# Optimization experiments

Measured on AMD Instinct MI355X. Metric: run time of the kernel, lower is better.

Reference implementation:

```python
import jax, jax.numpy as jnp
import numpy as np

N, K, CIN, COUT = 150000, 27, 128, 128


def setup_inputs() -> dict:
    key = jax.random.key(0)
    k1, k2, k3 = jax.random.split(key, 3)
    data = jax.random.normal(k1, (N, CIN), dtype=jnp.float32)
    weights = jax.random.normal(k2, (COUT, K, CIN), dtype=jnp.float32) * 0.05
    # neighbour indices in [-1, N): -1 marks empty octree neighbours (~1/151 here)
    neighbour = jax.random.randint(k3, (N, K), 0, N + 1, dtype=jnp.int64) - 1
    return {"data": data, "weights": weights, "neighbour": neighbour}


def reference(data, weights, neighbour):
    """Octree sparse conv: out[m] = sum_k W[:,k,:] @ data[neigh[m,k]] (0 if -1).

    Scans over the 27 kernel offsets so the [N,K,Cin] gather is never
    materialized; each step is a masked row-gather + dense GEMM.
    """
    w_k = jnp.transpose(weights, (1, 2, 0))   # [K, Cin, Cout]
    n_k = neighbour.T                          # [K, N]

    def body(acc, xs):
        w, idx = xs                            # [Cin, Cout], [N]
        valid = (idx >= 0)[:, None]            # [N, 1]
        g = jnp.where(valid, data[jnp.clip(idx, 0, None)], 0.0)  # [N, Cin]
        return acc + g @ w, None

    out0 = jnp.zeros((data.shape[0], w_k.shape[-1]), dtype=data.dtype)
    out, _ = jax.lax.scan(body, out0, (w_k, n_k))
    return out
```

## Files before the change

kernel.cpp:

```cpp
#include <hip/hip_runtime.h>

#define N_PTS 150000
#define NK 27
#define CIN 128
#define COUT 128
#define BM 128
#define NBLK ((N_PTS + BM - 1) / BM)

typedef __attribute__((ext_vector_type(8))) short bfrag8;
typedef __attribute__((ext_vector_type(4))) float facc4;

__device__ inline unsigned short f2bf(float f) {
    unsigned u = __builtin_bit_cast(unsigned, f);
    u += 0x7FFFu + ((u >> 16) & 1u);
    return (unsigned short)(u >> 16);
}
__device__ inline unsigned pack2(float a, float b) {
    return (unsigned)f2bf(a) | ((unsigned)f2bf(b) << 16);
}
__device__ inline void glds16(const void* g, void* l) {
    __builtin_amdgcn_global_load_lds(
        (const __attribute__((address_space(1))) void*)g,
        (__attribute__((address_space(3))) void*)l, 16, 0, 0);
}

__global__ void cast_data_kernel(const float* __restrict__ in,
                                 unsigned short* __restrict__ out) {
    const int n8_data = N_PTS * (CIN / 8);
    const int n8_all  = (N_PTS + 1) * (CIN / 8);
    int i = blockIdx.x * blockDim.x + threadIdx.x;
    int stride = gridDim.x * blockDim.x;
    for (; i < n8_all; i += stride) {
        uint4 v;
        if (i < n8_data) {
            const float4* p = (const float4*)(in + (size_t)i * 8);
            float4 x = p[0], y = p[1];
            v.x = pack2(x.x, x.y); v.y = pack2(x.z, x.w);
            v.z = pack2(y.x, y.y); v.w = pack2(y.z, y.w);
        } else {
            v.x = v.y = v.z = v.w = 0u;
        }
        *(uint4*)(out + (size_t)i * 8) = v;
    }
}

__global__ void prep_weights_h(const float* __restrict__ w,
                               unsigned short* __restrict__ wkh) {
    int i = blockIdx.x * blockDim.x + threadIdx.x;
    if (i >= NK * 2 * 128 * 8) return;
    int bu = i & 7, co = (i >> 3) & 127, h = (i >> 10) & 1, k = i >> 11;
    int ci = h * 64 + (bu ^ (co & 7)) * 8;
    const float4* src = (const float4*)(w + ((size_t)co * NK + k) * CIN + ci);
    float4 x = src[0], y = src[1];
    uint4 v;
    v.x = pack2(x.x, x.y); v.y = pack2(x.z, x.w);
    v.z = pack2(y.x, y.y); v.w = pack2(y.z, y.w);
    ((uint4*)wkh)[i] = v;
}


#define STAGE_A(Q, ADST)                                                     \
  {                                                                          \
    const int k_  = (Q) >> 1;                                                \
    const int hb_ = ((Q) & 1) << 7;                                          \
    int iv0 = *(const int*)(ldsI + s0 * 108 + k_ * 4);                       \
    int iv1 = *(const int*)(ldsI + s1 * 108 + k_ * 4);                       \
    size_t e0 = (s0ok && iv0 >= 0) ? (size_t)iv0 : (size_t)N_PTS;            \
    size_t e1 = (s1ok && iv1 >= 0) ? (size_t)iv1 : (size_t)N_PTS;            \
    glds16(dbfB + e0 * 256 + hb_ + aswz, (ADST) + s0 * 128 + lu16);          \
    glds16(dbfB + e1 * 256 + hb_ + aswz, (ADST) + s1 * 128 + lu16);          \
  }

#define STAGE_B(Q, BDST)                                                     \
  {                                                                          \
    const char* bs_ = wkhB + (size_t)(Q) * 16384 + t * 16;                   \
    glds16(bs_,        (BDST) + t * 16);                                     \
    glds16(bs_ + 8192, (BDST) + t * 16 + 8192);                              \
  }

#define MFMA_PHASE(ABUF, BBUF)                                                      \
  {                                                                                 \
    __builtin_amdgcn_s_setprio(1);                                                  \
    _Pragma("unroll")                                                               \
    for (int kk = 0; kk < 2; ++kk) {                                                \
      const int sw_ = (((kk * 4 + lk) ^ (lr & 7)) << 4);                            \
      bfrag8 a0 = *(const bfrag8*)((ABUF) + (wrow * 32 + lr) * 128 + sw_);          \
      bfrag8 a1 = *(const bfrag8*)((ABUF) + (wrow * 32 + 16 + lr) * 128 + sw_);     \
      _Pragma("unroll")                                                             \
      for (int ct = 0; ct < 4; ++ct) {                                              \
        bfrag8 b = *(const bfrag8*)((BBUF) + (h * 64 + ct * 16 + lr) * 128 + sw_);  \
        acc[0][ct] = __builtin_amdgcn_mfma_f32_16x16x32_bf16(a0, b, acc[0][ct],     \
                                                             0, 0, 0);              \
        acc[1][ct] = __builtin_amdgcn_mfma_f32_16x16x32_bf16(a1, b, acc[1][ct],     \
                                                             0, 0, 0);              \
      }                                                                             \
    }                                                                               \
    __builtin_amdgcn_s_setprio(0);                                                  \
  }

#define WAIT_BAR(N)                                                          \
    __builtin_amdgcn_sched_barrier(0);                                       \
    asm volatile("s_waitcnt vmcnt(" #N ")" ::: "memory");                    \
    __builtin_amdgcn_s_barrier();                                            \
    __builtin_amdgcn_sched_barrier(0);

__global__ __launch_bounds__(512, 4)
void octconv_v10(const unsigned short* __restrict__ dbf,
                 const unsigned short* __restrict__ wkh,
                 const int* __restrict__ nbr,
                 float* __restrict__ out) {
    __shared__ __align__(1024) unsigned char lds[2 * 16384 + 2 * 16384 + 13824];

    const int t = threadIdx.x;
    const int w = t >> 6, l = t & 63;
    const int lr = l & 15, lk = l >> 4;
    const int h = w & 1, wrow = w >> 1;
    const int m0 = blockIdx.x * BM;

    const int lu   = l & 7;
    const int lu16 = lu * 16;
    const int s0 = t >> 3;
    const int s1 = s0 + 64;
    const bool s0ok = (m0 + s0) < N_PTS;
    const bool s1ok = (m0 + s1) < N_PTS;
    const int aswz = (lu ^ (s0 & 7)) << 4;

    const char* dbfB = (const char*)dbf;
    const char* wkhB = (const char*)wkh;
    char* a0p = (char*)lds;
    char* a1p = (char*)lds + 16384;
    char* b0p = (char*)lds + 32768;
    char* b1p = (char*)lds + 49152;
    char* ldsI = (char*)lds + 65536;

    facc4 acc[2][4];
    const facc4 fz = {0.f, 0.f, 0.f, 0.f};
#pragma unroll
    for (int a = 0; a < 2; ++a)
#pragma unroll
        for (int b = 0; b < 4; ++b) acc[a][b] = fz;

    {
        const char* nsrc = (const char*)nbr + (size_t)m0 * 108;
        const int rows_valid = (N_PTS - m0) < BM ? (N_PTS - m0) : BM;
        const int nlimit = rows_valid * 108;
        int o;
        o = t * 16;        if (o < nlimit) glds16(nsrc + o, ldsI + o);
        o = 8192 + t * 16; if (t < 352 && o < nlimit) glds16(nsrc + o, ldsI + o);
    }
    WAIT_BAR(0)

    STAGE_A(0, a0p)
    STAGE_B(0, b0p)
    WAIT_BAR(0)

#pragma unroll 1
    for (int p = 0; p <= 52; ++p) {
        STAGE_B(p + 1, b1p)
        STAGE_A(p + 1, a1p)
        MFMA_PHASE(a0p, b0p)
        WAIT_BAR(0)
        { char* tp = a0p; a0p = a1p; a1p = tp; }
        { char* tp = b0p; b0p = b1p; b1p = tp; }
    }

    MFMA_PHASE(a0p, b0p)

#pragma unroll
    for (int rt = 0; rt < 2; ++rt) {
        const int r0 = m0 + wrow * 32 + rt * 16 + lk * 4;
#pragma unroll
        for (int ct = 0; ct < 4; ++ct) {
#pragma unroll
            for (int r = 0; r < 4; ++r) {
                int row = r0 + r;
                if (row < N_PTS)
                    out[(size_t)row * COUT + h * 64 + ct * 16 + lr] = acc[rt][ct][r];
            }
        }
    }
}

__global__ void naive_kernel(const float* __restrict__ data, const float* __restrict__ wgt,
                             const int* __restrict__ nbr, float* __restrict__ out) {
    int mm = blockIdx.x;
    int co = threadIdx.x;
    if (mm >= N_PTS) return;
    float acc = 0.f;
    for (int k = 0; k < NK; ++k) {
        int idx = nbr[mm * NK + k];
        if (idx < 0) continue;
        const float* d  = data + (size_t)idx * CIN;
        const float* wp = wgt + ((size_t)co * NK + k) * CIN;
        for (int ci = 0; ci < CIN; ++ci) acc += d[ci] * wp[ci];
    }
    out[(size_t)mm * COUT + co] = acc;
}

extern "C" void kernel_launch(void* const* d_in, const int* in_sizes, int n_in,
                              void* d_out, int out_size, void* d_ws, size_t ws_size,
                              hipStream_t stream) {
    const float* data = (const float*)d_in[0];
    const float* wgt  = (const float*)d_in[1];
    const int*   nbr  = (const int*)d_in[2];
    float*       out  = (float*)d_out;

    const size_t wk_bytes  = (size_t)NK * 2 * 128 * 8 * 16;
    const size_t dbf_bytes = (size_t)(N_PTS + 1) * CIN * 2;

    if (ws_size < wk_bytes + dbf_bytes) {
        naive_kernel<<<N_PTS, COUT, 0, stream>>>(data, wgt, nbr, out);
        return;
    }
    unsigned short* wkh = (unsigned short*)d_ws;
    unsigned short* dbf = (unsigned short*)((char*)d_ws + wk_bytes);

    prep_weights_h<<<(NK * 2 * 128 * 8 + 255) / 256, 256, 0, stream>>>(wgt, wkh);
    cast_data_kernel<<<2048, 256, 0, stream>>>(data, dbf);

    octconv_v10<<<NBLK, 512, 0, stream>>>(dbf, wkh, nbr, out);
}
```

Measured before the change: 189.0 us.

## Halve block to 256 threads with 64x64 warp tiles for more B-fragment reuse

Each block now runs 4 waves instead of 8, and each wave computes a 64-row by 64-column output tile (4x4 MFMA accumulators) instead of 32x64. Every B fragment read from LDS feeds four MFMAs instead of two, which cuts LDS read traffic per MFMA. Staging of A, B and the neighbour indices is remapped so fewer threads issue more loads each. In exchange each wave uses more accumulator registers, and there are fewer waves per block to hide gather latency.

```diff
diff --git a/kernel.cpp b/kernel.cpp
--- a/kernel.cpp
+++ b/kernel.cpp
@@ -63,19 +63,20 @@
   {                                                                          \
     const int k_  = (Q) >> 1;                                                \
     const int hb_ = ((Q) & 1) << 7;                                          \
-    int iv0 = *(const int*)(ldsI + s0 * 108 + k_ * 4);                       \
-    int iv1 = *(const int*)(ldsI + s1 * 108 + k_ * 4);                       \
-    size_t e0 = (s0ok && iv0 >= 0) ? (size_t)iv0 : (size_t)N_PTS;            \
-    size_t e1 = (s1ok && iv1 >= 0) ? (size_t)iv1 : (size_t)N_PTS;            \
-    glds16(dbfB + e0 * 256 + hb_ + aswz, (ADST) + s0 * 128 + lu16);          \
-    glds16(dbfB + e1 * 256 + hb_ + aswz, (ADST) + s1 * 128 + lu16);          \
+    _Pragma("unroll")                                                        \
+    for (int j_ = 0; j_ < 4; ++j_) {                                         \
+      int iv = *(const int*)(ldsI + (sbase + j_ * 32) * 108 + k_ * 4);       \
+      size_t e = (sok[j_] && iv >= 0) ? (size_t)iv : (size_t)N_PTS;          \
+      glds16(dbfB + e * 256 + hb_ + aswz, (ADST) + j_ * 4096 + w * 1024);    \
+    }                                                                        \
   }
 
 #define STAGE_B(Q, BDST)                                                     \
   {                                                                          \
-    const char* bs_ = wkhB + (size_t)(Q) * 16384 + t * 16;                   \
-    glds16(bs_,        (BDST) + t * 16);                                     \
-    glds16(bs_ + 8192, (BDST) + t * 16 + 8192);                              \
+    const char* bs_ = wkhB + (size_t)(Q) * 16384 + w * 4096 + l * 16;        \
+    _Pragma("unroll")                                                        \
+    for (int j_ = 0; j_ < 4; ++j_)                                           \
+      glds16(bs_ + j_ * 1024, (BDST) + w * 4096 + j_ * 1024);                \
   }
 
 #define MFMA_PHASE(ABUF, BBUF)                                                      \
@@ -84,14 +85,20 @@
     _Pragma("unroll")                                                               \
     for (int kk = 0; kk < 2; ++kk) {                                                \
       const int sw_ = (((kk * 4 + lk) ^ (lr & 7)) << 4);                            \
-      bfrag8 a0 = *(const bfrag8*)((ABUF) + (wrow * 32 + lr) * 128 + sw_);          \
-      bfrag8 a1 = *(const bfrag8*)((ABUF) + (wrow * 32 + 16 + lr) * 128 + sw_);     \
+      bfrag8 a0 = *(const bfrag8*)((ABUF) + (wrow * 64 + lr) * 128 + sw_);          \
+      bfrag8 a1 = *(const bfrag8*)((ABUF) + (wrow * 64 + 16 + lr) * 128 + sw_);     \
+      bfrag8 a2 = *(const bfrag8*)((ABUF) + (wrow * 64 + 32 + lr) * 128 + sw_);     \
+      bfrag8 a3 = *(const bfrag8*)((ABUF) + (wrow * 64 + 48 + lr) * 128 + sw_);     \
       _Pragma("unroll")                                                             \
       for (int ct = 0; ct < 4; ++ct) {                                              \
         bfrag8 b = *(const bfrag8*)((BBUF) + (h * 64 + ct * 16 + lr) * 128 + sw_);  \
         acc[0][ct] = __builtin_amdgcn_mfma_f32_16x16x32_bf16(a0, b, acc[0][ct],     \
                                                              0, 0, 0);              \
         acc[1][ct] = __builtin_amdgcn_mfma_f32_16x16x32_bf16(a1, b, acc[1][ct],     \
+                                                             0, 0, 0);              \
+        acc[2][ct] = __builtin_amdgcn_mfma_f32_16x16x32_bf16(a2, b, acc[2][ct],     \
+                                                             0, 0, 0);              \
+        acc[3][ct] = __builtin_amdgcn_mfma_f32_16x16x32_bf16(a3, b, acc[3][ct],     \
                                                              0, 0, 0);              \
       }                                                                             \
     }                                                                               \
@@ -104,12 +111,12 @@
     __builtin_amdgcn_s_barrier();                                            \
     __builtin_amdgcn_sched_barrier(0);
 
-__global__ __launch_bounds__(512, 4)
-void octconv_v10(const unsigned short* __restrict__ dbf,
+__global__ __launch_bounds__(256, 2)
+void octconv_v14(const unsigned short* __restrict__ dbf,
                  const unsigned short* __restrict__ wkh,
                  const int* __restrict__ nbr,
                  float* __restrict__ out) {
-    __shared__ __align__(1024) unsigned char lds[2 * 16384 + 2 * 16384 + 13824];
+    __shared__ __align__(1024) unsigned char lds[4 * 16384 + 13824];
 
     const int t = threadIdx.x;
     const int w = t >> 6, l = t & 63;
@@ -118,25 +125,24 @@
     const int m0 = blockIdx.x * BM;
 
     const int lu   = l & 7;
-    const int lu16 = lu * 16;
-    const int s0 = t >> 3;
-    const int s1 = s0 + 64;
-    const bool s0ok = (m0 + s0) < N_PTS;
-    const bool s1ok = (m0 + s1) < N_PTS;
-    const int aswz = (lu ^ (s0 & 7)) << 4;
+    const int sbase = w * 8 + (l >> 3);
+    const int aswz  = (lu ^ (sbase & 7)) << 4;
+    bool sok[4];
+#pragma unroll
+    for (int j = 0; j < 4; ++j) sok[j] = (m0 + sbase + j * 32) < N_PTS;
 
     const char* dbfB = (const char*)dbf;
     const char* wkhB = (const char*)wkh;
-    char* a0p = (char*)lds;
-    char* a1p = (char*)lds + 16384;
-    char* b0p = (char*)lds + 32768;
-    char* b1p = (char*)lds + 49152;
+    char* pA0 = (char*)lds;
+    char* pA1 = (char*)lds + 16384;
+    char* pB0 = (char*)lds + 32768;
+    char* pB1 = (char*)lds + 49152;
     char* ldsI = (char*)lds + 65536;
 
-    facc4 acc[2][4];
+    facc4 acc[4][4];
     const facc4 fz = {0.f, 0.f, 0.f, 0.f};
 #pragma unroll
-    for (int a = 0; a < 2; ++a)
+    for (int a = 0; a < 4; ++a)
 #pragma unroll
         for (int b = 0; b < 4; ++b) acc[a][b] = fz;
 
@@ -145,30 +151,32 @@
         const int rows_valid = (N_PTS - m0) < BM ? (N_PTS - m0) : BM;
         const int nlimit = rows_valid * 108;
         int o;
-        o = t * 16;        if (o < nlimit) glds16(nsrc + o, ldsI + o);
-        o = 8192 + t * 16; if (t < 352 && o < nlimit) glds16(nsrc + o, ldsI + o);
+        o = t * 16;         if (o < nlimit) glds16(nsrc + o, ldsI + o);
+        o = 4096 + t * 16;  if (o < nlimit) glds16(nsrc + o, ldsI + o);
+        o = 8192 + t * 16;  if (o < nlimit) glds16(nsrc + o, ldsI + o);
+        o = 12288 + t * 16; if (t < 96 && o < nlimit) glds16(nsrc + o, ldsI + o);
     }
     WAIT_BAR(0)
 
-    STAGE_A(0, a0p)
-    STAGE_B(0, b0p)
+    STAGE_A(0, pA0)
+    STAGE_B(0, pB0)
     WAIT_BAR(0)
 
 #pragma unroll 1
     for (int p = 0; p <= 52; ++p) {
-        STAGE_B(p + 1, b1p)
-        STAGE_A(p + 1, a1p)
-        MFMA_PHASE(a0p, b0p)
+        STAGE_B(p + 1, pB1)
+        STAGE_A(p + 1, pA1)
+        MFMA_PHASE(pA0, pB0)
         WAIT_BAR(0)
-        { char* tp = a0p; a0p = a1p; a1p = tp; }
-        { char* tp = b0p; b0p = b1p; b1p = tp; }
-    }
-
-    MFMA_PHASE(a0p, b0p)
-
-#pragma unroll
-    for (int rt = 0; rt < 2; ++rt) {
-        const int r0 = m0 + wrow * 32 + rt * 16 + lk * 4;
+        { char* tp = pA0; pA0 = pA1; pA1 = tp; }
+        { char* tp = pB0; pB0 = pB1; pB1 = tp; }
+    }
+
+    MFMA_PHASE(pA0, pB0)
+
+#pragma unroll
+    for (int rt = 0; rt < 4; ++rt) {
+        const int r0 = m0 + wrow * 64 + rt * 16 + lk * 4;
 #pragma unroll
         for (int ct = 0; ct < 4; ++ct) {
 #pragma unroll
@@ -218,5 +226,5 @@
     prep_weights_h<<<(NK * 2 * 128 * 8 + 255) / 256, 256, 0, stream>>>(wgt, wkh);
     cast_data_kernel<<<2048, 256, 0, stream>>>(data, dbf);
 
-    octconv_v10<<<NBLK, 512, 0, stream>>>(dbf, wkh, nbr, out);
-}
+    octconv_v14<<<NBLK, 256, 0, stream>>>(dbf, wkh, nbr, out);
+}
```

Result: slower. 195.6 us (+3.5%).
